# Optimization experiments

Measured on AMD Instinct MI355X. Metric: run time of the kernel, lower is better.

## Reference

```python
import jax, jax.numpy as jnp
import numpy as np

C = 32        # channels per degree
NDEG = 4      # degrees 0..3
NLAYERS = 4   # hidden GSE3Res layers
OUTC = 64     # output fiber degree-0 channels
BATCH = 16
NPOINTS = 128
RBF_D = 16


def _sph(u):
    # real spherical harmonics l=0..3 on unit vectors u [E,3]
    x, y, z = u[:, 0], u[:, 1], u[:, 2]
    Y0 = 0.28209479177 * jnp.ones_like(x)[:, None]
    Y1 = 0.48860251190 * jnp.stack([y, z, x], -1)
    Y2 = jnp.stack([1.09254843059 * x * y, 1.09254843059 * y * z,
                    0.31539156525 * (3.0 * z * z - 1.0), 1.09254843059 * x * z,
                    0.54627421529 * (x * x - y * y)], -1)
    Y3 = jnp.stack([0.59004358992 * y * (3.0 * x * x - y * y), 2.89061144264 * x * y * z,
                    0.45704579946 * y * (5.0 * z * z - 1.0), 0.37317633259 * z * (5.0 * z * z - 3.0),
                    0.45704579946 * x * (5.0 * z * z - 1.0), 1.44530572132 * z * (x * x - y * y),
                    0.59004358992 * x * (x * x - 3.0 * y * y)], -1)
    return [Y0, Y1, Y2, Y3]


def _seg_softmax(logits, seg, n):
    m = jax.ops.segment_max(logits, seg, num_segments=n)
    e = jnp.exp(logits - m[seg])
    s = jax.ops.segment_sum(e, seg, num_segments=n)
    return e / s[seg]


def _forward(x, w1, b1, rW, sW, Wv, Wq, Wk, Wo, Wskip, gw, gb,
             w1o, b1o, roW, WvO, WqO, WkO, WoO, WskipO,
             Whid, bhid, Wout, bout, src, dst, gid):
    N = x.shape[0]
    rel = x[dst] - x[src]                                  # [E,3]
    d = jnp.sqrt((rel * rel).sum(-1) + 1e-12)              # [E]
    Ys = _sph(rel / d[:, None])
    centers = jnp.linspace(0.0, 4.0, RBF_D)
    rbf = jnp.exp(-((d[:, None] - centers) ** 2) / (2.0 * 0.5 ** 2))  # [E,16]
    # input fiber {1:1} is zeros_like(x) in the original -> start from zero features
    h = [jnp.zeros((N, C, 2 * l + 1), x.dtype) for l in range(NDEG)]
    for i in range(NLAYERS):
        rh = jax.nn.relu(rbf @ w1[i] + b1[i])              # [E,32] radial net
        q = h[0][:, :, 0] @ Wq[i]                          # [N,32] invariant query
        k = rh @ Wk[i]                                     # [E,32]
        logit = (q[dst] * k).sum(-1) / (C ** 0.5)
        alpha = _seg_softmax(logit, dst, N)
        h0s = h[0][src][:, :, 0]                           # [E,32]
        new = []
        for l in range(NDEG):
            hs = h[l][src]                                 # [E,C,2l+1]
            R = rh @ rW[i, l]                              # [E,C] same-degree radial gate
            S = rh @ sW[i, l]                              # [E,C] degree0->l path
            v = jnp.einsum('ecm,cd->edm', hs, Wv[i, l]) * R[:, :, None]
            v = v + (S * (h0s + 1.0))[:, :, None] * Ys[l][:, None, :]
            agg = jax.ops.segment_sum(alpha[:, None, None] * v, dst, num_segments=N)
            hn = (jnp.einsum('ncm,cd->ndm', h[l], Wskip[i, l])
                  + jnp.einsum('ncm,cd->ndm', agg, Wo[i, l]))
            # GNormBias: norm nonlinearity with learned scale/bias
            nrm = jnp.sqrt((hn * hn).sum(-1) + 1e-12)      # [N,C]
            phi = jax.nn.relu(nrm * gw[i, l] + gb[i, l])
            new.append(hn * (phi / (nrm + 1e-6))[:, :, None])
        h = new
    # final GSE3Res to degree-0 out fiber (64 channels)
    rh = jax.nn.relu(rbf @ w1o + b1o)
    q = h[0][:, :, 0] @ WqO                                # [N,64]
    k = rh @ WkO                                           # [E,64]
    logit = (q[dst] * k).sum(-1) / (OUTC ** 0.5)
    alpha = _seg_softmax(logit, dst, N)
    m0 = jnp.zeros((src.shape[0], OUTC), x.dtype)
    for l in range(NDEG):
        c = jnp.einsum('ecm,em->ec', h[l][src], Ys[l])     # invariant contraction
        m0 = m0 + (c @ WvO[l]) * (rh @ roW[l])
    agg = jax.ops.segment_sum(alpha[:, None] * m0, dst, num_segments=N)
    hout = agg @ WoO + h[0][:, :, 0] @ WskipO              # [N,64]
    # GAvgPooling per graph, then MLP head
    cnt = jax.ops.segment_sum(jnp.ones((N,), x.dtype), gid, num_segments=BATCH)
    pooled = jax.ops.segment_sum(hout, gid, num_segments=BATCH) / cnt[:, None]
    return jax.nn.relu(pooled @ Whid + bhid) @ Wout + bout  # [B,15]


def setup_inputs() -> dict:
    key = jax.random.key(0)
    ks = jax.random.split(key, 30)
    P, B = NPOINTS, BATCH
    N = B * P
    a = np.repeat(np.arange(P), P)
    b = np.tile(np.arange(P), P)
    m = a != b
    a, b = a[m], b[m]
    src = jnp.asarray(np.concatenate([a + g * P for g in range(B)]), jnp.int32)
    dst = jnp.asarray(np.concatenate([b + g * P for g in range(B)]), jnp.int32)
    gid = jnp.asarray(np.repeat(np.arange(B), P), jnp.int32)

    def w(k, shape, s=0.1):
        return (jax.random.normal(k, shape) * s).astype(jnp.float32)

    return {
        'x': jax.random.normal(ks[0], (N, 3), jnp.float32),
        'w1': w(ks[1], (4, 16, 32)), 'b1': w(ks[2], (4, 32)),
        'rW': w(ks[3], (4, 4, 32, 32)), 'sW': w(ks[4], (4, 4, 32, 32)),
        'Wv': w(ks[5], (4, 4, 32, 32)), 'Wq': w(ks[6], (4, 32, 32)), 'Wk': w(ks[7], (4, 32, 32)),
        'Wo': w(ks[8], (4, 4, 32, 32)), 'Wskip': w(ks[9], (4, 4, 32, 32)),
        'gw': w(ks[10], (4, 4, 32)), 'gb': w(ks[11], (4, 4, 32)) + 0.5,
        'w1o': w(ks[12], (16, 32)), 'b1o': w(ks[13], (32,)),
        'roW': w(ks[14], (4, 32, 64)), 'WvO': w(ks[15], (4, 32, 64)),
        'WqO': w(ks[16], (32, 64)), 'WkO': w(ks[17], (32, 64)),
        'WoO': w(ks[18], (64, 64)), 'WskipO': w(ks[19], (32, 64)),
        'Whid': w(ks[20], (64, 64)), 'bhid': w(ks[21], (64,)),
        'Wout': w(ks[22], (64, 15)), 'bout': w(ks[23], (15,)),
        'src': src, 'dst': dst, 'gid': gid,
    }


def reference(x, w1, b1, rW, sW, Wv, Wq, Wk, Wo, Wskip, gw, gb,
              w1o, b1o, roW, WvO, WqO, WkO, WoO, WskipO,
              Whid, bhid, Wout, bout, src, dst, gid):
    return _forward(x, w1, b1, rW, sW, Wv, Wq, Wk, Wo, Wskip, gw, gb,
                    w1o, b1o, roW, WvO, WqO, WkO, WoO, WskipO,
                    Whid, bhid, Wout, bout, src, dst, gid)
```

## Files before the change

kernel.cpp:

```cpp
#include <hip/hip_runtime.h>
#include <hip/hip_bf16.h>

#define NNODE 2048
#define NGRAPH 16

__device__ __forceinline__ int lmap(int m) { return m == 0 ? 0 : (m < 4 ? 1 : (m < 9 ? 2 : 3)); }

__device__ __forceinline__ float f4get(const float4& v, int j) {
    return j == 0 ? v.x : (j == 1 ? v.y : (j == 2 ? v.z : v.w));
}

__device__ __forceinline__ void sph16(float x, float y, float z, float* Y) {
    Y[0] = 0.28209479177f;
    Y[1] = 0.4886025119f * y; Y[2] = 0.4886025119f * z; Y[3] = 0.4886025119f * x;
    Y[4] = 1.09254843059f * x * y;
    Y[5] = 1.09254843059f * y * z;
    Y[6] = 0.31539156525f * (3.f * z * z - 1.f);
    Y[7] = 1.09254843059f * x * z;
    Y[8] = 0.54627421529f * (x * x - y * y);
    Y[9]  = 0.59004358992f * y * (3.f * x * x - y * y);
    Y[10] = 2.89061144264f * x * y * z;
    Y[11] = 0.45704579946f * y * (5.f * z * z - 1.f);
    Y[12] = 0.37317633259f * z * (5.f * z * z - 3.f);
    Y[13] = 0.45704579946f * x * (5.f * z * z - 1.f);
    Y[14] = 1.44530572132f * z * (x * x - y * y);
    Y[15] = 0.59004358992f * x * (x * x - 3.f * y * y);
}

__global__ __launch_bounds__(256, 2) void k_layer(
    const float* __restrict__ x, const float* __restrict__ h,
    const float* __restrict__ vpre, const float* __restrict__ wqk,
    const float* __restrict__ w1, const float* __restrict__ b1,
    const float* __restrict__ rW, const float* __restrict__ sW,
    const float* __restrict__ Wskip, const float* __restrict__ Wo,
    const float* __restrict__ gw, const float* __restrict__ gb,
    const float* __restrict__ Wv_n, const float* __restrict__ Wq_n, const float* __restrict__ Wk_n,
    const float* __restrict__ WvO, const float* __restrict__ WqO, const float* __restrict__ WkO,
    float* __restrict__ hnew, float* __restrict__ vpre_n, float* __restrict__ wqk_n,
    float* __restrict__ wq2, float* __restrict__ U,
    int layer, int last)
{
    __shared__ __align__(16) float rwsw[8192];
    __shared__ __align__(16) float rhs[128 * 36];
    __shared__ __align__(16) float yss[128 * 17];
    __shared__ __align__(16) float hnS[528];
    __shared__ __align__(16) float aggL[528];
    __shared__ float xs[384];
    __shared__ float w1s[512];
    __shared__ float b1s[32];
    __shared__ float wqks[32];
    __shared__ float alphas[128];
    __shared__ float red[256];
    __shared__ float scale[128];
    __shared__ float sh_inv;

    int n = blockIdx.x, t = threadIdx.x;
    int g = n >> 7, b = n & 127;
    int gbase = g << 7;

    for (int o = t; o < 384; o += 256) xs[o] = x[gbase * 3 + o];
    for (int o = t; o < 512; o += 256) w1s[o] = w1[layer * 512 + o];
    if (t < 32) { b1s[t] = b1[layer * 32 + t]; wqks[t] = wqk[n * 32 + t]; }
    for (int o = t; o < 4096; o += 256) {
        rwsw[o * 2] = rW[layer * 4096 + o];
        rwsw[o * 2 + 1] = sW[layer * 4096 + o];
    }
    __syncthreads();

    if (t < 128) {
        int a = t;
        float rx = xs[b * 3 + 0] - xs[a * 3 + 0];
        float ry = xs[b * 3 + 1] - xs[a * 3 + 1];
        float rz = xs[b * 3 + 2] - xs[a * 3 + 2];
        float dd = sqrtf(rx * rx + ry * ry + rz * rz + 1e-12f);
        float inv = 1.f / dd;
        float ys[16];
        sph16(rx * inv, ry * inv, rz * inv, ys);
#pragma unroll
        for (int m = 0; m < 16; m++) yss[a * 17 + m] = ys[m];
        float rbf[16];
#pragma unroll
        for (int j = 0; j < 16; j++) {
            float dc = dd - (4.f / 15.f) * j;
            rbf[j] = __expf(-2.f * dc * dc);
        }
        float logit = 0.f;
        for (int d = 0; d < 32; d++) {
            float s = b1s[d];
#pragma unroll
            for (int j = 0; j < 16; j++) s = fmaf(rbf[j], w1s[j * 32 + d], s);
            s = fmaxf(s, 0.f);
            rhs[a * 36 + d] = s;
            logit = fmaf(s, wqks[d], logit);
        }
        alphas[a] = logit * 0.17677669529663687f;
    }
    __syncthreads();

    red[t] = (t < 128 && t != b) ? alphas[t] : -1e30f;
    __syncthreads();
    for (int s2 = 128; s2 > 0; s2 >>= 1) { if (t < s2) red[t] = fmaxf(red[t], red[t + s2]); __syncthreads(); }
    float mx = red[0];
    __syncthreads();
    float e = (t < 128 && t != b) ? __expf(alphas[t] - mx) : 0.f;
    red[t] = e;
    __syncthreads();
    for (int s2 = 128; s2 > 0; s2 >>= 1) { if (t < s2) red[t] += red[t + s2]; __syncthreads(); }
    if (t == 0) sh_inv = 1.f / red[0];
    if (t < 128) alphas[t] = e;
    __syncthreads();

    int grp = t >> 5, d = t & 31;
    float acc[16];
#pragma unroll
    for (int m = 0; m < 16; m++) acc[m] = 0.f;

    for (int chunk = 0; chunk < 2; chunk++) {
        int a0 = grp * 16 + chunk * 8;
        float R[8][4], S[8][4];
#pragma unroll
        for (int aa = 0; aa < 8; aa++)
#pragma unroll
            for (int l = 0; l < 4; l++) { R[aa][l] = 0.f; S[aa][l] = 0.f; }

#pragma unroll 2
        for (int jq = 0; jq < 8; jq++) {
            float4 rh4[8];
#pragma unroll
            for (int aa = 0; aa < 8; aa++)
                rh4[aa] = *reinterpret_cast<const float4*>(&rhs[(a0 + aa) * 36 + jq * 4]);
#pragma unroll
            for (int l = 0; l < 4; l++) {
#pragma unroll
                for (int jj = 0; jj < 4; jj++) {
                    float2 w2 = *reinterpret_cast<const float2*>(&rwsw[((l * 32 + jq * 4 + jj) * 32 + d) * 2]);
#pragma unroll
                    for (int aa = 0; aa < 8; aa++) {
                        float rv = f4get(rh4[aa], jj);
                        R[aa][l] = fmaf(rv, w2.x, R[aa][l]);
                        S[aa][l] = fmaf(rv, w2.y, S[aa][l]);
                    }
                }
            }
        }

        int nb = (gbase + a0) * 512 + d * 16;
        const float4* vp4 = reinterpret_cast<const float4*>(vpre + nb);
        float4 u0 = vp4[0], u1 = vp4[1], u2 = vp4[2], u3 = vp4[3];
        float h0v = h[nb];
#pragma unroll
        for (int aa = 0; aa < 8; aa++) {
            float4 n0 = u0, n1 = u1, n2 = u2, n3 = u3; float nh = h0v;
            if (aa < 7) {
                int nb2 = (gbase + a0 + aa + 1) * 512 + d * 16;
                const float4* np4 = reinterpret_cast<const float4*>(vpre + nb2);
                n0 = np4[0]; n1 = np4[1]; n2 = np4[2]; n3 = np4[3];
                nh = h[nb2];
            }
            int a = a0 + aa;
            float w = alphas[a];
            if (w != 0.f) {
                const float* ysa = &yss[a * 17];
                float hb1 = h0v + 1.f;
                float sc0 = S[aa][0] * hb1, sc1 = S[aa][1] * hb1;
                float sc2 = S[aa][2] * hb1, sc3 = S[aa][3] * hb1;
                acc[0]  = fmaf(w, fmaf(u0.x, R[aa][0], sc0 * ysa[0]),  acc[0]);
                acc[1]  = fmaf(w, fmaf(u0.y, R[aa][1], sc1 * ysa[1]),  acc[1]);
                acc[2]  = fmaf(w, fmaf(u0.z, R[aa][1], sc1 * ysa[2]),  acc[2]);
                acc[3]  = fmaf(w, fmaf(u0.w, R[aa][1], sc1 * ysa[3]),  acc[3]);
                acc[4]  = fmaf(w, fmaf(u1.x, R[aa][2], sc2 * ysa[4]),  acc[4]);
                acc[5]  = fmaf(w, fmaf(u1.y, R[aa][2], sc2 * ysa[5]),  acc[5]);
                acc[6]  = fmaf(w, fmaf(u1.z, R[aa][2], sc2 * ysa[6]),  acc[6]);
                acc[7]  = fmaf(w, fmaf(u1.w, R[aa][2], sc2 * ysa[7]),  acc[7]);
                acc[8]  = fmaf(w, fmaf(u2.x, R[aa][2], sc2 * ysa[8]),  acc[8]);
                acc[9]  = fmaf(w, fmaf(u2.y, R[aa][3], sc3 * ysa[9]),  acc[9]);
                acc[10] = fmaf(w, fmaf(u2.z, R[aa][3], sc3 * ysa[10]), acc[10]);
                acc[11] = fmaf(w, fmaf(u2.w, R[aa][3], sc3 * ysa[11]), acc[11]);
                acc[12] = fmaf(w, fmaf(u3.x, R[aa][3], sc3 * ysa[12]), acc[12]);
                acc[13] = fmaf(w, fmaf(u3.y, R[aa][3], sc3 * ysa[13]), acc[13]);
                acc[14] = fmaf(w, fmaf(u3.z, R[aa][3], sc3 * ysa[14]), acc[14]);
                acc[15] = fmaf(w, fmaf(u3.w, R[aa][3], sc3 * ysa[15]), acc[15]);
            }
            u0 = n0; u1 = n1; u2 = n2; u3 = n3; h0v = nh;
        }
    }
    __syncthreads();

    float* P = rhs;
#pragma unroll
    for (int m = 0; m < 16; m++) P[grp * 528 + m * 33 + d] = acc[m];
    float* hs = yss;
    for (int o = t; o < 512; o += 256) hs[o] = h[n * 512 + o];
    for (int o = t; o < 4096; o += 256) {
        rwsw[o] = Wskip[layer * 4096 + o];
        rwsw[4096 + o] = Wo[layer * 4096 + o];
    }
    __syncthreads();

    float invs = sh_inv;
    for (int o = t; o < 512; o += 256) {
        int m = o >> 5, c = o & 31;
        float s = 0.f;
#pragma unroll
        for (int gg = 0; gg < 8; gg++) s += P[gg * 528 + m * 33 + c];
        aggL[m * 33 + c] = s * invs;
    }
    __syncthreads();

    for (int o = t; o < 512; o += 256) {
        int m = o >> 5, dd = o & 31, l = lmap(m);
        float s = 0.f;
        const float* wa = &rwsw[l * 1024 + dd];
        const float* wb = &rwsw[4096 + l * 1024 + dd];
        const float* hrow = &hs[m];
        const float* arow = &aggL[m * 33];
#pragma unroll
        for (int c = 0; c < 32; c++) {
            s = fmaf(hrow[c * 16], wa[c * 32], s);
            s = fmaf(arow[c],      wb[c * 32], s);
        }
        hnS[m * 33 + dd] = s;
    }
    __syncthreads();

    if (t < 128) {
        int dd = t >> 2, l = t & 3;
        int m0 = l * l, cnt = 2 * l + 1;
        float s = 1e-12f;
        for (int m = m0; m < m0 + cnt; m++) { float v = hnS[m * 33 + dd]; s = fmaf(v, v, s); }
        float nr = sqrtf(s);
        float phi = fmaxf(nr * gw[(layer * 4 + l) * 32 + dd] + gb[(layer * 4 + l) * 32 + dd], 0.f);
        scale[dd * 4 + l] = phi / (nr + 1e-6f);
    }
    __syncthreads();

    for (int o = t; o < 512; o += 256) {
        int dd = o >> 4, m = o & 15;
        float v = hnS[m * 33 + dd] * scale[dd * 4 + lmap(m)];
        hnew[n * 512 + o] = v;
        hnS[m * 33 + dd] = v;
    }
    int wsz = last ? 8192 : 4096;
    for (int o = t; o < wsz; o += 256) rwsw[o] = last ? WvO[o] : Wv_n[o];
    __syncthreads();

    if (!last) {
        for (int o = t; o < 512; o += 256) {
            int dd = o >> 4, m = o & 15, l = lmap(m);
            float s = 0.f;
            const float* wv = &rwsw[l * 1024 + dd];
            const float* hrow = &hnS[m * 33];
#pragma unroll
            for (int c = 0; c < 32; c++) s = fmaf(hrow[c], wv[c * 32], s);
            vpre_n[n * 512 + o] = s;
        }
        if (t < 32) {
            float s = 0.f;
#pragma unroll
            for (int c = 0; c < 32; c++) s = fmaf(hnS[c], Wq_n[c * 32 + t], s);
            red[t] = s;
        }
        __syncthreads();
        if (t < 32) {
            float s = 0.f;
#pragma unroll
            for (int j = 0; j < 32; j++) s = fmaf(Wk_n[t * 32 + j], red[j], s);
            wqk_n[n * 32 + t] = s;
        }
    } else {
        for (int o = t; o < 1024; o += 256) {
            int j = o >> 4, m = o & 15, l = lmap(m);
            float s = 0.f;
            const float* wv = &rwsw[l * 2048 + j];
            const float* hrow = &hnS[m * 33];
#pragma unroll
            for (int c = 0; c < 32; c++) s = fmaf(hrow[c], wv[c * 64], s);
            U[n * 1024 + o] = s;
        }
        if (t < 64) {
            float s = 0.f;
#pragma unroll
            for (int c = 0; c < 32; c++) s = fmaf(hnS[c], WqO[c * 64 + t], s);
            red[t] = s;
        }
        __syncthreads();
        if (t < 32) {
            float s = 0.f;
#pragma unroll
            for (int j = 0; j < 64; j++) s = fmaf(WkO[t * 64 + j], red[j], s);
            wq2[n * 32 + t] = s;
        }
    }
}

__global__ __launch_bounds__(256, 2) void k_out_edge(
    const float* __restrict__ x, const float* __restrict__ h,
    const float* __restrict__ w1o, const float* __restrict__ b1o,
    const float* __restrict__ wq2, const float* __restrict__ roW,
    const float* __restrict__ U, const float* __restrict__ WoO,
    const float* __restrict__ WskipO, float* __restrict__ hout)
{
    __shared__ __align__(16) float ros[8192];
    __shared__ __align__(16) float rhs[128 * 36];
    __shared__ __align__(16) float yss[128 * 17];
    __shared__ float xs[384];
    __shared__ float w1s[512];
    __shared__ float b1s[32];
    __shared__ float wq2s[32];
    __shared__ float alphas[128];
    __shared__ float red[256];
    __shared__ float agg64s[64];
    __shared__ float sh_inv;

    int n = blockIdx.x, t = threadIdx.x;
    int g = n >> 7, b = n & 127;
    int gbase = g << 7;

    for (int o = t; o < 384; o += 256) xs[o] = x[gbase * 3 + o];
    for (int o = t; o < 512; o += 256) w1s[o] = w1o[o];
    if (t < 32) { b1s[t] = b1o[t]; wq2s[t] = wq2[n * 32 + t]; }
    for (int o = t; o < 8192; o += 256) ros[o] = roW[o];
    __syncthreads();

    if (t < 128) {
        int a = t;
        float rx = xs[b * 3 + 0] - xs[a * 3 + 0];
        float ry = xs[b * 3 + 1] - xs[a * 3 + 1];
        float rz = xs[b * 3 + 2] - xs[a * 3 + 2];
        float dd = sqrtf(rx * rx + ry * ry + rz * rz + 1e-12f);
        float inv = 1.f / dd;
        float ys[16];
        sph16(rx * inv, ry * inv, rz * inv, ys);
#pragma unroll
        for (int m = 0; m < 16; m++) yss[a * 17 + m] = ys[m];
        float rbf[16];
#pragma unroll
        for (int j = 0; j < 16; j++) {
            float dc = dd - (4.f / 15.f) * j;
            rbf[j] = __expf(-2.f * dc * dc);
        }
        float logit = 0.f;
        for (int d = 0; d < 32; d++) {
            float s = b1s[d];
#pragma unroll
            for (int j = 0; j < 16; j++) s = fmaf(rbf[j], w1s[j * 32 + d], s);
            s = fmaxf(s, 0.f);
            rhs[a * 36 + d] = s;
            logit = fmaf(s, wq2s[d], logit);
        }
        alphas[a] = logit * 0.125f;
    }
    __syncthreads();

    red[t] = (t < 128 && t != b) ? alphas[t] : -1e30f;
    __syncthreads();
    for (int s2 = 128; s2 > 0; s2 >>= 1) { if (t < s2) red[t] = fmaxf(red[t], red[t + s2]); __syncthreads(); }
    float mx = red[0];
    __syncthreads();
    float e = (t < 128 && t != b) ? __expf(alphas[t] - mx) : 0.f;
    red[t] = e;
    __syncthreads();
    for (int s2 = 128; s2 > 0; s2 >>= 1) { if (t < s2) red[t] += red[t + s2]; __syncthreads(); }
    if (t == 0) sh_inv = 1.f / red[0];
    if (t < 128) alphas[t] = e;
    __syncthreads();

    int grp = t >> 6, j = t & 63;
    float accO = 0.f;
    for (int chunk = 0; chunk < 4; chunk++) {
        int a0 = grp * 32 + chunk * 8;
        float RO[8][4];
#pragma unroll
        for (int aa = 0; aa < 8; aa++)
#pragma unroll
            for (int l = 0; l < 4; l++) RO[aa][l] = 0.f;

#pragma unroll 2
        for (int cq = 0; cq < 8; cq++) {
            float4 rh4[8];
#pragma unroll
            for (int aa = 0; aa < 8; aa++)
                rh4[aa] = *reinterpret_cast<const float4*>(&rhs[(a0 + aa) * 36 + cq * 4]);
#pragma unroll
            for (int l = 0; l < 4; l++) {
#pragma unroll
                for (int cc = 0; cc < 4; cc++) {
                    float wv = ros[(l * 32 + cq * 4 + cc) * 64 + j];
#pragma unroll
                    for (int aa = 0; aa < 8; aa++)
                        RO[aa][l] = fmaf(f4get(rh4[aa], cc), wv, RO[aa][l]);
                }
            }
        }

        const float4* Up = reinterpret_cast<const float4*>(U + (gbase + a0) * 1024 + j * 16);
        float4 u0 = Up[0], u1 = Up[1], u2 = Up[2], u3 = Up[3];
#pragma unroll
        for (int aa = 0; aa < 8; aa++) {
            float4 n0 = u0, n1 = u1, n2 = u2, n3 = u3;
            if (aa < 7) {
                const float4* Np = reinterpret_cast<const float4*>(U + (gbase + a0 + aa + 1) * 1024 + j * 16);
                n0 = Np[0]; n1 = Np[1]; n2 = Np[2]; n3 = Np[3];
            }
            int a = a0 + aa;
            float w = alphas[a];
            if (w != 0.f) {
                const float* ysa = &yss[a * 17];
                float cv0 = ysa[0] * u0.x;
                float cv1 = fmaf(ysa[1], u0.y, fmaf(ysa[2], u0.z, ysa[3] * u0.w));
                float cv2 = fmaf(ysa[4], u1.x, fmaf(ysa[5], u1.y, fmaf(ysa[6], u1.z, fmaf(ysa[7], u1.w, ysa[8] * u2.x))));
                float cv3 = fmaf(ysa[9], u2.y, fmaf(ysa[10], u2.z, fmaf(ysa[11], u2.w,
                            fmaf(ysa[12], u3.x, fmaf(ysa[13], u3.y, fmaf(ysa[14], u3.z, ysa[15] * u3.w))))));
                float s = fmaf(cv0, RO[aa][0], fmaf(cv1, RO[aa][1], fmaf(cv2, RO[aa][2], cv3 * RO[aa][3])));
                accO = fmaf(w, s, accO);
            }
            u0 = n0; u1 = n1; u2 = n2; u3 = n3;
        }
    }
    red[t] = accO;
    __syncthreads();
    if (t < 64) agg64s[t] = (red[t] + red[64 + t] + red[128 + t] + red[192 + t]) * sh_inv;
    __syncthreads();

    if (t < 64) {
        float s = 0.f;
#pragma unroll
        for (int c = 0; c < 64; c++) s = fmaf(agg64s[c], WoO[c * 64 + t], s);
        const float* hr = &h[n * 512];
#pragma unroll
        for (int c = 0; c < 32; c++) s = fmaf(hr[c * 16], WskipO[c * 64 + t], s);
        hout[n * 64 + t] = s;
    }
}

__global__ __launch_bounds__(64) void k_final(
    const float* __restrict__ hout, const float* __restrict__ Whid,
    const float* __restrict__ bhid, const float* __restrict__ Wout,
    const float* __restrict__ bout, float* __restrict__ out)
{
    __shared__ float pooled[64], hid[64];
    int g = blockIdx.x, t = threadIdx.x;
    float s = 0.f;
    for (int p = 0; p < 128; p++) s += hout[(g * 128 + p) * 64 + t];
    pooled[t] = s * (1.f / 128.f);
    __syncthreads();
    float hv = bhid[t];
#pragma unroll
    for (int c = 0; c < 64; c++) hv = fmaf(pooled[c], Whid[c * 64 + t], hv);
    hid[t] = fmaxf(hv, 0.f);
    __syncthreads();
    if (t < 15) {
        float o = bout[t];
#pragma unroll
        for (int c = 0; c < 64; c++) o = fmaf(hid[c], Wout[c * 15 + t], o);
        out[g * 15 + t] = o;
    }
}

extern "C" void kernel_launch(void* const* d_in, const int* in_sizes, int n_in,
                              void* d_out, int out_size, void* d_ws, size_t ws_size,
                              hipStream_t stream) {
    const float* x      = (const float*)d_in[0];
    const float* w1     = (const float*)d_in[1];
    const float* b1     = (const float*)d_in[2];
    const float* rW     = (const float*)d_in[3];
    const float* sW     = (const float*)d_in[4];
    const float* Wv     = (const float*)d_in[5];
    const float* Wq     = (const float*)d_in[6];
    const float* Wk     = (const float*)d_in[7];
    const float* Wo     = (const float*)d_in[8];
    const float* Wskip  = (const float*)d_in[9];
    const float* gw     = (const float*)d_in[10];
    const float* gb     = (const float*)d_in[11];
    const float* w1o    = (const float*)d_in[12];
    const float* b1o    = (const float*)d_in[13];
    const float* roW    = (const float*)d_in[14];
    const float* WvO    = (const float*)d_in[15];
    const float* WqO    = (const float*)d_in[16];
    const float* WkO    = (const float*)d_in[17];
    const float* WoO    = (const float*)d_in[18];
    const float* WskipO = (const float*)d_in[19];
    const float* Whid   = (const float*)d_in[20];
    const float* bhid   = (const float*)d_in[21];
    const float* Wout   = (const float*)d_in[22];
    const float* bout   = (const float*)d_in[23];
    float* out = (float*)d_out;

    float* ws = (float*)d_ws;
    float* h0    = ws;
    float* h1    = h0 + NNODE * 512;
    float* vA    = h1 + NNODE * 512;
    float* wqkA  = vA + NNODE * 512;
    float* vB    = wqkA + NNODE * 32;
    float* wqkB  = vB + NNODE * 512;
    float* wq2   = wqkB + NNODE * 32;
    float* U     = wq2 + NNODE * 32;
    float* hout  = U + NNODE * 1024;

    hipMemsetAsync(h0, 0, NNODE * 512 * sizeof(float), stream);
    hipMemsetAsync(vA, 0, (NNODE * 512 + NNODE * 32) * sizeof(float), stream);

    for (int i = 0; i < 4; i++) {
        const float* hc  = (i & 1) ? h1 : h0;
        float*       hn  = (i & 1) ? h0 : h1;
        const float* vin  = (i & 1) ? vB : vA;
        const float* qin  = (i & 1) ? wqkB : wqkA;
        float*       vout = (i & 1) ? vA : vB;
        float*       qout = (i & 1) ? wqkA : wqkB;
        int last = (i == 3);
        k_layer<<<NNODE, 256, 0, stream>>>(
            x, hc, vin, qin, w1, b1, rW, sW, Wskip, Wo, gw, gb,
            Wv + (last ? 0 : (i + 1) * 4096),
            Wq + (last ? 0 : (i + 1) * 1024),
            Wk + (last ? 0 : (i + 1) * 1024),
            WvO, WqO, WkO,
            hn, vout, qout, wq2, U, i, last);
    }
    k_out_edge<<<NNODE, 256, 0, stream>>>(x, h0, w1o, b1o, wq2, roW, U, WoO, WskipO, hout);
    k_out_post_unused: ;
    k_final<<<NGRAPH, 64, 0, stream>>>(hout, Whid, bhid, Wout, bout, out);
}
```

Measured before the change: 638.0 us.

## Pack radial weights as fp16 pairs in LDS and raise occupancy to 3 blocks

The radial weight tables rW/sW (and roW in the output kernel) are now stored in shared memory as packed half2 pairs, which halves that buffer. Several shared arrays are aliased onto reused buffers so LDS per block shrinks, and launch bounds rise to allow 3 blocks per CU. The radial-net setup is split across all 256 threads instead of 128, and the gather loop is double-buffered with two prefetch streams. The fp16 weights lose precision and could move outputs past tolerance, and tighter register limits may cause spills.

```diff
diff --git a/kernel.cpp b/kernel.cpp
--- a/kernel.cpp
+++ b/kernel.cpp
@@ -1,5 +1,6 @@
 #include <hip/hip_runtime.h>
 #include <hip/hip_bf16.h>
+#include <hip/hip_fp16.h>
 
 #define NNODE 2048
 #define NGRAPH 16
@@ -8,6 +9,15 @@
 
 __device__ __forceinline__ float f4get(const float4& v, int j) {
     return j == 0 ? v.x : (j == 1 ? v.y : (j == 2 ? v.z : v.w));
+}
+
+__device__ __forceinline__ uint32_t f2h2(float a, float b) {
+    __half2 h2 = __floats2half2_rn(a, b);
+    return *reinterpret_cast<uint32_t*>(&h2);
+}
+__device__ __forceinline__ float2 h2f2(uint32_t u) {
+    __half2 h2 = *reinterpret_cast<__half2*>(&u);
+    return __half22float2(h2);
 }
 
 __device__ __forceinline__ void sph16(float x, float y, float z, float* Y) {
@@ -27,7 +37,33 @@
     Y[15] = 0.59004358992f * x * (x * x - 3.f * y * y);
 }
 
-__global__ __launch_bounds__(256, 2) void k_layer(
+#define PROC_SRC(aa, u0, u1, u2, u3, h0v) { \
+    int a_ = a0 + (aa); \
+    float w_ = alphas[a_]; \
+    if (w_ != 0.f) { \
+        const float* ysa = &yss[a_ * 17]; \
+        float hb1 = (h0v) + 1.f; \
+        float sc0 = S[aa][0] * hb1, sc1 = S[aa][1] * hb1; \
+        float sc2 = S[aa][2] * hb1, sc3 = S[aa][3] * hb1; \
+        acc[0]  = fmaf(w_, fmaf((u0).x, R[aa][0], sc0 * ysa[0]),  acc[0]); \
+        acc[1]  = fmaf(w_, fmaf((u0).y, R[aa][1], sc1 * ysa[1]),  acc[1]); \
+        acc[2]  = fmaf(w_, fmaf((u0).z, R[aa][1], sc1 * ysa[2]),  acc[2]); \
+        acc[3]  = fmaf(w_, fmaf((u0).w, R[aa][1], sc1 * ysa[3]),  acc[3]); \
+        acc[4]  = fmaf(w_, fmaf((u1).x, R[aa][2], sc2 * ysa[4]),  acc[4]); \
+        acc[5]  = fmaf(w_, fmaf((u1).y, R[aa][2], sc2 * ysa[5]),  acc[5]); \
+        acc[6]  = fmaf(w_, fmaf((u1).z, R[aa][2], sc2 * ysa[6]),  acc[6]); \
+        acc[7]  = fmaf(w_, fmaf((u1).w, R[aa][2], sc2 * ysa[7]),  acc[7]); \
+        acc[8]  = fmaf(w_, fmaf((u2).x, R[aa][2], sc2 * ysa[8]),  acc[8]); \
+        acc[9]  = fmaf(w_, fmaf((u2).y, R[aa][3], sc3 * ysa[9]),  acc[9]); \
+        acc[10] = fmaf(w_, fmaf((u2).z, R[aa][3], sc3 * ysa[10]), acc[10]); \
+        acc[11] = fmaf(w_, fmaf((u2).w, R[aa][3], sc3 * ysa[11]), acc[11]); \
+        acc[12] = fmaf(w_, fmaf((u3).x, R[aa][3], sc3 * ysa[12]), acc[12]); \
+        acc[13] = fmaf(w_, fmaf((u3).y, R[aa][3], sc3 * ysa[13]), acc[13]); \
+        acc[14] = fmaf(w_, fmaf((u3).z, R[aa][3], sc3 * ysa[14]), acc[14]); \
+        acc[15] = fmaf(w_, fmaf((u3).w, R[aa][3], sc3 * ysa[15]), acc[15]); \
+    } }
+
+__global__ __launch_bounds__(256, 3) void k_layer(
     const float* __restrict__ x, const float* __restrict__ h,
     const float* __restrict__ vpre, const float* __restrict__ wqk,
     const float* __restrict__ w1, const float* __restrict__ b1,
@@ -40,13 +76,10 @@
     float* __restrict__ wq2, float* __restrict__ U,
     int layer, int last)
 {
-    __shared__ __align__(16) float rwsw[8192];
+    __shared__ uint32_t rwswP[4096];
     __shared__ __align__(16) float rhs[128 * 36];
     __shared__ __align__(16) float yss[128 * 17];
-    __shared__ __align__(16) float hnS[528];
-    __shared__ __align__(16) float aggL[528];
-    __shared__ float xs[384];
-    __shared__ float w1s[512];
+    __shared__ __align__(16) float ub[1056];
     __shared__ float b1s[32];
     __shared__ float wqks[32];
     __shared__ float alphas[128];
@@ -58,17 +91,18 @@
     int g = n >> 7, b = n & 127;
     int gbase = g << 7;
 
+    float* xs = ub;
+    float* w1s = ub + 384;
+
     for (int o = t; o < 384; o += 256) xs[o] = x[gbase * 3 + o];
     for (int o = t; o < 512; o += 256) w1s[o] = w1[layer * 512 + o];
     if (t < 32) { b1s[t] = b1[layer * 32 + t]; wqks[t] = wqk[n * 32 + t]; }
-    for (int o = t; o < 4096; o += 256) {
-        rwsw[o * 2] = rW[layer * 4096 + o];
-        rwsw[o * 2 + 1] = sW[layer * 4096 + o];
-    }
-    __syncthreads();
-
-    if (t < 128) {
-        int a = t;
+    for (int o = t; o < 4096; o += 256)
+        rwswP[o] = f2h2(rW[layer * 4096 + o], sW[layer * 4096 + o]);
+    __syncthreads();
+
+    {
+        int a = t & 127, dh = t >> 7;
         float rx = xs[b * 3 + 0] - xs[a * 3 + 0];
         float ry = xs[b * 3 + 1] - xs[a * 3 + 1];
         float rz = xs[b * 3 + 2] - xs[a * 3 + 2];
@@ -76,25 +110,31 @@
         float inv = 1.f / dd;
         float ys[16];
         sph16(rx * inv, ry * inv, rz * inv, ys);
-#pragma unroll
-        for (int m = 0; m < 16; m++) yss[a * 17 + m] = ys[m];
+        if (dh == 0) {
+#pragma unroll
+            for (int m = 0; m < 16; m++) yss[a * 17 + m] = ys[m];
+        }
         float rbf[16];
 #pragma unroll
         for (int j = 0; j < 16; j++) {
             float dc = dd - (4.f / 15.f) * j;
             rbf[j] = __expf(-2.f * dc * dc);
         }
-        float logit = 0.f;
-        for (int d = 0; d < 32; d++) {
+        float lpart = 0.f;
+        int d0 = dh * 16;
+        for (int d2 = 0; d2 < 16; d2++) {
+            int d = d0 + d2;
             float s = b1s[d];
 #pragma unroll
             for (int j = 0; j < 16; j++) s = fmaf(rbf[j], w1s[j * 32 + d], s);
             s = fmaxf(s, 0.f);
             rhs[a * 36 + d] = s;
-            logit = fmaf(s, wqks[d], logit);
-        }
-        alphas[a] = logit * 0.17677669529663687f;
-    }
+            lpart = fmaf(s, wqks[d], lpart);
+        }
+        red[t] = lpart;
+    }
+    __syncthreads();
+    if (t < 128) alphas[t] = (red[t] + red[t + 128]) * 0.17677669529663687f;
     __syncthreads();
 
     red[t] = (t < 128 && t != b) ? alphas[t] : -1e30f;
@@ -133,7 +173,7 @@
             for (int l = 0; l < 4; l++) {
 #pragma unroll
                 for (int jj = 0; jj < 4; jj++) {
-                    float2 w2 = *reinterpret_cast<const float2*>(&rwsw[((l * 32 + jq * 4 + jj) * 32 + d) * 2]);
+                    float2 w2 = h2f2(rwswP[(l * 32 + jq * 4 + jj) * 32 + d]);
 #pragma unroll
                     for (int aa = 0; aa < 8; aa++) {
                         float rv = f4get(rh4[aa], jj);
@@ -144,44 +184,36 @@
             }
         }
 
-        int nb = (gbase + a0) * 512 + d * 16;
-        const float4* vp4 = reinterpret_cast<const float4*>(vpre + nb);
-        float4 u0 = vp4[0], u1 = vp4[1], u2 = vp4[2], u3 = vp4[3];
-        float h0v = h[nb];
-#pragma unroll
-        for (int aa = 0; aa < 8; aa++) {
-            float4 n0 = u0, n1 = u1, n2 = u2, n3 = u3; float nh = h0v;
-            if (aa < 7) {
-                int nb2 = (gbase + a0 + aa + 1) * 512 + d * 16;
-                const float4* np4 = reinterpret_cast<const float4*>(vpre + nb2);
-                n0 = np4[0]; n1 = np4[1]; n2 = np4[2]; n3 = np4[3];
-                nh = h[nb2];
-            }
-            int a = a0 + aa;
-            float w = alphas[a];
-            if (w != 0.f) {
-                const float* ysa = &yss[a * 17];
-                float hb1 = h0v + 1.f;
-                float sc0 = S[aa][0] * hb1, sc1 = S[aa][1] * hb1;
-                float sc2 = S[aa][2] * hb1, sc3 = S[aa][3] * hb1;
-                acc[0]  = fmaf(w, fmaf(u0.x, R[aa][0], sc0 * ysa[0]),  acc[0]);
-                acc[1]  = fmaf(w, fmaf(u0.y, R[aa][1], sc1 * ysa[1]),  acc[1]);
-                acc[2]  = fmaf(w, fmaf(u0.z, R[aa][1], sc1 * ysa[2]),  acc[2]);
-                acc[3]  = fmaf(w, fmaf(u0.w, R[aa][1], sc1 * ysa[3]),  acc[3]);
-                acc[4]  = fmaf(w, fmaf(u1.x, R[aa][2], sc2 * ysa[4]),  acc[4]);
-                acc[5]  = fmaf(w, fmaf(u1.y, R[aa][2], sc2 * ysa[5]),  acc[5]);
-                acc[6]  = fmaf(w, fmaf(u1.z, R[aa][2], sc2 * ysa[6]),  acc[6]);
-                acc[7]  = fmaf(w, fmaf(u1.w, R[aa][2], sc2 * ysa[7]),  acc[7]);
-                acc[8]  = fmaf(w, fmaf(u2.x, R[aa][2], sc2 * ysa[8]),  acc[8]);
-                acc[9]  = fmaf(w, fmaf(u2.y, R[aa][3], sc3 * ysa[9]),  acc[9]);
-                acc[10] = fmaf(w, fmaf(u2.z, R[aa][3], sc3 * ysa[10]), acc[10]);
-                acc[11] = fmaf(w, fmaf(u2.w, R[aa][3], sc3 * ysa[11]), acc[11]);
-                acc[12] = fmaf(w, fmaf(u3.x, R[aa][3], sc3 * ysa[12]), acc[12]);
-                acc[13] = fmaf(w, fmaf(u3.y, R[aa][3], sc3 * ysa[13]), acc[13]);
-                acc[14] = fmaf(w, fmaf(u3.z, R[aa][3], sc3 * ysa[14]), acc[14]);
-                acc[15] = fmaf(w, fmaf(u3.w, R[aa][3], sc3 * ysa[15]), acc[15]);
-            }
-            u0 = n0; u1 = n1; u2 = n2; u3 = n3; h0v = nh;
+        float4 A0, A1, A2, A3, B0, B1, B2, B3; float Ah, Bh;
+        {
+            int nb = (gbase + a0) * 512 + d * 16;
+            const float4* p4 = reinterpret_cast<const float4*>(vpre + nb);
+            A0 = p4[0]; A1 = p4[1]; A2 = p4[2]; A3 = p4[3]; Ah = h[nb];
+            int nb2 = (gbase + a0 + 1) * 512 + d * 16;
+            const float4* q4 = reinterpret_cast<const float4*>(vpre + nb2);
+            B0 = q4[0]; B1 = q4[1]; B2 = q4[2]; B3 = q4[3]; Bh = h[nb2];
+        }
+#pragma unroll
+        for (int ap = 0; ap < 4; ap++) {
+            int aa = ap * 2;
+            {
+                float4 u0 = A0, u1 = A1, u2 = A2, u3 = A3; float h0v = Ah;
+                if (ap < 3) {
+                    int nb2 = (gbase + a0 + aa + 2) * 512 + d * 16;
+                    const float4* p4 = reinterpret_cast<const float4*>(vpre + nb2);
+                    A0 = p4[0]; A1 = p4[1]; A2 = p4[2]; A3 = p4[3]; Ah = h[nb2];
+                }
+                PROC_SRC(aa, u0, u1, u2, u3, h0v)
+            }
+            {
+                float4 u0 = B0, u1 = B1, u2 = B2, u3 = B3; float h0v = Bh;
+                if (ap < 3) {
+                    int nb2 = (gbase + a0 + aa + 3) * 512 + d * 16;
+                    const float4* p4 = reinterpret_cast<const float4*>(vpre + nb2);
+                    B0 = p4[0]; B1 = p4[1]; B2 = p4[2]; B3 = p4[3]; Bh = h[nb2];
+                }
+                PROC_SRC(aa + 1, u0, u1, u2, u3, h0v)
+            }
         }
     }
     __syncthreads();
@@ -191,12 +223,11 @@
     for (int m = 0; m < 16; m++) P[grp * 528 + m * 33 + d] = acc[m];
     float* hs = yss;
     for (int o = t; o < 512; o += 256) hs[o] = h[n * 512 + o];
-    for (int o = t; o < 4096; o += 256) {
-        rwsw[o] = Wskip[layer * 4096 + o];
-        rwsw[4096 + o] = Wo[layer * 4096 + o];
-    }
-    __syncthreads();
-
+    for (int o = t; o < 4096; o += 256) rwswP[o] = __float_as_uint(Wo[layer * 4096 + o]);
+    __syncthreads();
+
+    float* hnS = ub;
+    float* aggL = ub + 528;
     float invs = sh_inv;
     for (int o = t; o < 512; o += 256) {
         int m = o >> 5, c = o & 31;
@@ -207,17 +238,20 @@
     }
     __syncthreads();
 
+    for (int o = t; o < 4096; o += 256) rhs[o] = Wskip[layer * 4096 + o];
+    __syncthreads();
+
     for (int o = t; o < 512; o += 256) {
         int m = o >> 5, dd = o & 31, l = lmap(m);
         float s = 0.f;
-        const float* wa = &rwsw[l * 1024 + dd];
-        const float* wb = &rwsw[4096 + l * 1024 + dd];
+        const float* wa = &rhs[l * 1024 + dd];
+        const uint32_t* wb = &rwswP[l * 1024 + dd];
         const float* hrow = &hs[m];
         const float* arow = &aggL[m * 33];
 #pragma unroll
         for (int c = 0; c < 32; c++) {
             s = fmaf(hrow[c * 16], wa[c * 32], s);
-            s = fmaf(arow[c],      wb[c * 32], s);
+            s = fmaf(arow[c], __uint_as_float(wb[c * 32]), s);
         }
         hnS[m * 33 + dd] = s;
     }
@@ -232,6 +266,14 @@
         float phi = fmaxf(nr * gw[(layer * 4 + l) * 32 + dd] + gb[(layer * 4 + l) * 32 + dd], 0.f);
         scale[dd * 4 + l] = phi / (nr + 1e-6f);
     }
+    if (!last) {
+        for (int o = t; o < 4096; o += 256) rwswP[o] = __float_as_uint(Wv_n[o]);
+    } else {
+        for (int o = t; o < 4096; o += 256) {
+            rhs[o] = WvO[o];
+            rwswP[o] = __float_as_uint(WvO[4096 + o]);
+        }
+    }
     __syncthreads();
 
     for (int o = t; o < 512; o += 256) {
@@ -240,24 +282,22 @@
         hnew[n * 512 + o] = v;
         hnS[m * 33 + dd] = v;
     }
-    int wsz = last ? 8192 : 4096;
-    for (int o = t; o < wsz; o += 256) rwsw[o] = last ? WvO[o] : Wv_n[o];
     __syncthreads();
 
     if (!last) {
         for (int o = t; o < 512; o += 256) {
             int dd = o >> 4, m = o & 15, l = lmap(m);
             float s = 0.f;
-            const float* wv = &rwsw[l * 1024 + dd];
+            const uint32_t* wv = &rwswP[l * 1024 + dd];
             const float* hrow = &hnS[m * 33];
 #pragma unroll
-            for (int c = 0; c < 32; c++) s = fmaf(hrow[c], wv[c * 32], s);
+            for (int c = 0; c < 32; c++) s = fmaf(hrow[c], __uint_as_float(wv[c * 32]), s);
             vpre_n[n * 512 + o] = s;
         }
         if (t < 32) {
             float s = 0.f;
 #pragma unroll
-            for (int c = 0; c < 32; c++) s = fmaf(hnS[c], Wq_n[c * 32 + t], s);
+            for (int c = 0; c < 32; c++) s = fmaf(hnS[c * 33], Wq_n[c * 32 + t], s);
             red[t] = s;
         }
         __syncthreads();
@@ -271,16 +311,22 @@
         for (int o = t; o < 1024; o += 256) {
             int j = o >> 4, m = o & 15, l = lmap(m);
             float s = 0.f;
-            const float* wv = &rwsw[l * 2048 + j];
             const float* hrow = &hnS[m * 33];
-#pragma unroll
-            for (int c = 0; c < 32; c++) s = fmaf(hrow[c], wv[c * 64], s);
+            if (l < 2) {
+                const float* wv = &rhs[l * 2048 + j];
+#pragma unroll
+                for (int c = 0; c < 32; c++) s = fmaf(hrow[c], wv[c * 64], s);
+            } else {
+                const uint32_t* wv = &rwswP[(l - 2) * 2048 + j];
+#pragma unroll
+                for (int c = 0; c < 32; c++) s = fmaf(hrow[c], __uint_as_float(wv[c * 64]), s);
+            }
             U[n * 1024 + o] = s;
         }
         if (t < 64) {
             float s = 0.f;
 #pragma unroll
-            for (int c = 0; c < 32; c++) s = fmaf(hnS[c], WqO[c * 64 + t], s);
+            for (int c = 0; c < 32; c++) s = fmaf(hnS[c * 33], WqO[c * 64 + t], s);
             red[t] = s;
         }
         __syncthreads();
@@ -293,14 +339,14 @@
     }
 }
 
-__global__ __launch_bounds__(256, 2) void k_out_edge(
+__global__ __launch_bounds__(256, 3) void k_out_edge(
     const float* __restrict__ x, const float* __restrict__ h,
     const float* __restrict__ w1o, const float* __restrict__ b1o,
     const float* __restrict__ wq2, const float* __restrict__ roW,
     const float* __restrict__ U, const float* __restrict__ WoO,
     const float* __restrict__ WskipO, float* __restrict__ hout)
 {
-    __shared__ __align__(16) float ros[8192];
+    __shared__ uint32_t rosP[4096];
     __shared__ __align__(16) float rhs[128 * 36];
     __shared__ __align__(16) float yss[128 * 17];
     __shared__ float xs[384];
@@ -319,11 +365,14 @@
     for (int o = t; o < 384; o += 256) xs[o] = x[gbase * 3 + o];
     for (int o = t; o < 512; o += 256) w1s[o] = w1o[o];
     if (t < 32) { b1s[t] = b1o[t]; wq2s[t] = wq2[n * 32 + t]; }
-    for (int o = t; o < 8192; o += 256) ros[o] = roW[o];
-    __syncthreads();
-
-    if (t < 128) {
-        int a = t;
+    for (int o = t; o < 4096; o += 256) {
+        int j = o & 63, lc = o >> 6, cp = lc & 15, l = lc >> 4;
+        rosP[o] = f2h2(roW[(l * 32 + 2 * cp) * 64 + j], roW[(l * 32 + 2 * cp + 1) * 64 + j]);
+    }
+    __syncthreads();
+
+    {
+        int a = t & 127, dh = t >> 7;
         float rx = xs[b * 3 + 0] - xs[a * 3 + 0];
         float ry = xs[b * 3 + 1] - xs[a * 3 + 1];
         float rz = xs[b * 3 + 2] - xs[a * 3 + 2];
@@ -331,25 +380,31 @@
         float inv = 1.f / dd;
         float ys[16];
         sph16(rx * inv, ry * inv, rz * inv, ys);
-#pragma unroll
-        for (int m = 0; m < 16; m++) yss[a * 17 + m] = ys[m];
+        if (dh == 0) {
+#pragma unroll
+            for (int m = 0; m < 16; m++) yss[a * 17 + m] = ys[m];
+        }
         float rbf[16];
 #pragma unroll
         for (int j = 0; j < 16; j++) {
             float dc = dd - (4.f / 15.f) * j;
             rbf[j] = __expf(-2.f * dc * dc);
         }
-        float logit = 0.f;
-        for (int d = 0; d < 32; d++) {
+        float lpart = 0.f;
+        int d0 = dh * 16;
+        for (int d2 = 0; d2 < 16; d2++) {
+            int d = d0 + d2;
             float s = b1s[d];
 #pragma unroll
             for (int j = 0; j < 16; j++) s = fmaf(rbf[j], w1s[j * 32 + d], s);
             s = fmaxf(s, 0.f);
             rhs[a * 36 + d] = s;
-            logit = fmaf(s, wq2s[d], logit);
-        }
-        alphas[a] = logit * 0.125f;
-    }
+            lpart = fmaf(s, wq2s[d], lpart);
+        }
+        red[t] = lpart;
+    }
+    __syncthreads();
+    if (t < 128) alphas[t] = (red[t] + red[t + 128]) * 0.125f;
     __syncthreads();
 
     red[t] = (t < 128 && t != b) ? alphas[t] : -1e30f;
@@ -384,38 +439,58 @@
 #pragma unroll
             for (int l = 0; l < 4; l++) {
 #pragma unroll
-                for (int cc = 0; cc < 4; cc++) {
-                    float wv = ros[(l * 32 + cq * 4 + cc) * 64 + j];
-#pragma unroll
-                    for (int aa = 0; aa < 8; aa++)
-                        RO[aa][l] = fmaf(f4get(rh4[aa], cc), wv, RO[aa][l]);
+                for (int ch = 0; ch < 2; ch++) {
+                    float2 w2 = h2f2(rosP[(l * 16 + cq * 2 + ch) * 64 + j]);
+#pragma unroll
+                    for (int aa = 0; aa < 8; aa++) {
+                        RO[aa][l] = fmaf(f4get(rh4[aa], 2 * ch), w2.x, RO[aa][l]);
+                        RO[aa][l] = fmaf(f4get(rh4[aa], 2 * ch + 1), w2.y, RO[aa][l]);
+                    }
                 }
             }
         }
 
-        const float4* Up = reinterpret_cast<const float4*>(U + (gbase + a0) * 1024 + j * 16);
-        float4 u0 = Up[0], u1 = Up[1], u2 = Up[2], u3 = Up[3];
-#pragma unroll
-        for (int aa = 0; aa < 8; aa++) {
-            float4 n0 = u0, n1 = u1, n2 = u2, n3 = u3;
-            if (aa < 7) {
-                const float4* Np = reinterpret_cast<const float4*>(U + (gbase + a0 + aa + 1) * 1024 + j * 16);
-                n0 = Np[0]; n1 = Np[1]; n2 = Np[2]; n3 = Np[3];
-            }
-            int a = a0 + aa;
-            float w = alphas[a];
-            if (w != 0.f) {
-                const float* ysa = &yss[a * 17];
-                float cv0 = ysa[0] * u0.x;
-                float cv1 = fmaf(ysa[1], u0.y, fmaf(ysa[2], u0.z, ysa[3] * u0.w));
-                float cv2 = fmaf(ysa[4], u1.x, fmaf(ysa[5], u1.y, fmaf(ysa[6], u1.z, fmaf(ysa[7], u1.w, ysa[8] * u2.x))));
-                float cv3 = fmaf(ysa[9], u2.y, fmaf(ysa[10], u2.z, fmaf(ysa[11], u2.w,
-                            fmaf(ysa[12], u3.x, fmaf(ysa[13], u3.y, fmaf(ysa[14], u3.z, ysa[15] * u3.w))))));
-                float s = fmaf(cv0, RO[aa][0], fmaf(cv1, RO[aa][1], fmaf(cv2, RO[aa][2], cv3 * RO[aa][3])));
-                accO = fmaf(w, s, accO);
-            }
-            u0 = n0; u1 = n1; u2 = n2; u3 = n3;
-        }
+        float4 A0, A1, A2, A3, B0, B1, B2, B3;
+        {
+            const float4* p4 = reinterpret_cast<const float4*>(U + (gbase + a0) * 1024 + j * 16);
+            A0 = p4[0]; A1 = p4[1]; A2 = p4[2]; A3 = p4[3];
+            const float4* q4 = reinterpret_cast<const float4*>(U + (gbase + a0 + 1) * 1024 + j * 16);
+            B0 = q4[0]; B1 = q4[1]; B2 = q4[2]; B3 = q4[3];
+        }
+#define PROC_O(aa, u0, u1, u2, u3) { \
+        int a_ = a0 + (aa); \
+        float w_ = alphas[a_]; \
+        if (w_ != 0.f) { \
+            const float* ysa = &yss[a_ * 17]; \
+            float cv0 = ysa[0] * (u0).x; \
+            float cv1 = fmaf(ysa[1], (u0).y, fmaf(ysa[2], (u0).z, ysa[3] * (u0).w)); \
+            float cv2 = fmaf(ysa[4], (u1).x, fmaf(ysa[5], (u1).y, fmaf(ysa[6], (u1).z, fmaf(ysa[7], (u1).w, ysa[8] * (u2).x)))); \
+            float cv3 = fmaf(ysa[9], (u2).y, fmaf(ysa[10], (u2).z, fmaf(ysa[11], (u2).w, \
+                        fmaf(ysa[12], (u3).x, fmaf(ysa[13], (u3).y, fmaf(ysa[14], (u3).z, ysa[15] * (u3).w)))))); \
+            float s_ = fmaf(cv0, RO[aa][0], fmaf(cv1, RO[aa][1], fmaf(cv2, RO[aa][2], cv3 * RO[aa][3]))); \
+            accO = fmaf(w_, s_, accO); \
+        } }
+#pragma unroll
+        for (int ap = 0; ap < 4; ap++) {
+            int aa = ap * 2;
+            {
+                float4 u0 = A0, u1 = A1, u2 = A2, u3 = A3;
+                if (ap < 3) {
+                    const float4* p4 = reinterpret_cast<const float4*>(U + (gbase + a0 + aa + 2) * 1024 + j * 16);
+                    A0 = p4[0]; A1 = p4[1]; A2 = p4[2]; A3 = p4[3];
+                }
+                PROC_O(aa, u0, u1, u2, u3)
+            }
+            {
+                float4 u0 = B0, u1 = B1, u2 = B2, u3 = B3;
+                if (ap < 3) {
+                    const float4* p4 = reinterpret_cast<const float4*>(U + (gbase + a0 + aa + 3) * 1024 + j * 16);
+                    B0 = p4[0]; B1 = p4[1]; B2 = p4[2]; B3 = p4[3];
+                }
+                PROC_O(aa + 1, u0, u1, u2, u3)
+            }
+        }
+#undef PROC_O
     }
     red[t] = accO;
     __syncthreads();
@@ -517,6 +592,5 @@
             hn, vout, qout, wq2, U, i, last);
     }
     k_out_edge<<<NNODE, 256, 0, stream>>>(x, h0, w1o, b1o, wq2, roW, U, WoO, WskipO, hout);
-    k_out_post_unused: ;
     k_final<<<NGRAPH, 64, 0, stream>>>(hout, Whid, bhid, Wout, bout, out);
 }
```

Measured after the change: 601.0 us. -5.8%, faster.
